# Kernel tuning notes

Hardware: AMD Instinct MI355X
Metric: run time of the kernel (lower is better)

## Reference

```python
import jax, jax.numpy as jnp
import numpy as np

HEAD_DIM = 64
NUM_Q_HEADS = 32
NUM_KV_HEADS = 8
ROPE_FREQ = 10000.0
EPS = 1e-6


def _rms_norm(x, gamma):
    # normalize over last dim (head_dim)
    var = jnp.mean(jnp.square(x), axis=-1, keepdims=True)
    return x * jax.lax.rsqrt(var + EPS) * gamma


def _rope_cos_sin(seq_len, dtype=jnp.float32):
    inv_freq = 1.0 / (ROPE_FREQ ** (jnp.arange(0, HEAD_DIM, 2, dtype=jnp.float32) / HEAD_DIM))
    pos = jnp.arange(seq_len, dtype=jnp.float32)
    freqs = pos[:, None] * inv_freq[None, :]          # [S, hd/2]
    emb = jnp.concatenate([freqs, freqs], axis=-1)    # [S, hd]
    return jnp.cos(emb).astype(dtype), jnp.sin(emb).astype(dtype)


def _rotate_half(x):
    x1, x2 = jnp.split(x, 2, axis=-1)
    return jnp.concatenate([-x2, x1], axis=-1)


def _apply_rope(x, cos, sin):
    # x: [B, H, S, hd]; cos/sin: [S, hd]
    return x * cos[None, None, :, :] + _rotate_half(x) * sin[None, None, :, :]


def setup_inputs() -> dict:
    key = jax.random.key(0)
    ks = jax.random.split(key, 5)
    B, S, D = 2, 2048, 2048
    qkv_out = (NUM_Q_HEADS + 2 * NUM_KV_HEADS) * HEAD_DIM  # 3072
    x = jax.random.normal(ks[0], (B, S, D), dtype=jnp.float32)
    w_qkv = jax.random.normal(ks[1], (qkv_out, D), dtype=jnp.float32) * (D ** -0.5)
    w_out = jax.random.normal(ks[2], (D, NUM_Q_HEADS * HEAD_DIM), dtype=jnp.float32) * ((NUM_Q_HEADS * HEAD_DIM) ** -0.5)
    q_gamma = jnp.ones((HEAD_DIM,), dtype=jnp.float32)
    k_gamma = jnp.ones((HEAD_DIM,), dtype=jnp.float32)
    return {"x": x, "w_qkv": w_qkv, "w_out": w_out, "q_gamma": q_gamma, "k_gamma": k_gamma}


def reference(x, w_qkv, w_out, q_gamma, k_gamma):
    B, S, D = x.shape
    groups = NUM_Q_HEADS // NUM_KV_HEADS
    # fused QKV projection (no bias)
    qkv = jnp.einsum("bsd,od->bso", x, w_qkv)
    qkv = qkv.reshape(B, S, NUM_Q_HEADS + 2 * NUM_KV_HEADS, HEAD_DIM)
    qkv = jnp.transpose(qkv, (0, 2, 1, 3))  # [B, heads, S, hd]
    q = qkv[:, :NUM_Q_HEADS]
    k = qkv[:, NUM_Q_HEADS:NUM_Q_HEADS + NUM_KV_HEADS]
    v = qkv[:, NUM_Q_HEADS + NUM_KV_HEADS:]
    # QK RMSNorm over head_dim
    q = _rms_norm(q, q_gamma)
    k = _rms_norm(k, k_gamma)
    # RoPE
    cos, sin = _rope_cos_sin(S, dtype=x.dtype)
    q = _apply_rope(q, cos, sin)
    k = _apply_rope(k, cos, sin)
    # GQA: repeat-interleave kv heads
    k = jnp.repeat(k, groups, axis=1)
    v = jnp.repeat(v, groups, axis=1)
    # causal SDPA
    scale = HEAD_DIM ** -0.5
    scores = jnp.einsum("bhqd,bhkd->bhqk", q, k) * scale
    causal = jnp.tril(jnp.ones((S, S), dtype=bool))
    scores = jnp.where(causal[None, None], scores, jnp.finfo(scores.dtype).min)
    attn = jax.nn.softmax(scores, axis=-1)
    ctx = jnp.einsum("bhqk,bhkd->bhqd", attn, v)
    ctx = jnp.transpose(ctx, (0, 2, 1, 3)).reshape(B, S, NUM_Q_HEADS * HEAD_DIM)
    out = jnp.einsum("bsf,df->bsd", ctx, w_out)
    return out
```

## Files before the change

kernel.cpp:

```cpp
#include <hip/hip_runtime.h>

typedef _Float16 f16;
typedef __fp16 fp16x2 __attribute__((ext_vector_type(2)));
typedef _Float16 f16x8 __attribute__((ext_vector_type(8)));
typedef float f32x4 __attribute__((ext_vector_type(4)));
typedef float f32x16 __attribute__((ext_vector_type(16)));

#define AS1 __attribute__((address_space(1)))
#define AS3 __attribute__((address_space(3)))

#define SCALE_L2E 0.18033688011112042f


__device__ __forceinline__ void gload16(const void* g, void* l) {
    __builtin_amdgcn_global_load_lds(
        (const AS1 unsigned*)(unsigned long long)g,
        (AS3 unsigned*)(unsigned)(unsigned long long)l,
        16, 0, 0);
}

__device__ __forceinline__ unsigned pk2(float a, float b) {
    union { fp16x2 v; unsigned u; } c;
    c.v = __builtin_amdgcn_cvt_pkrtz(a, b);
    return c.u;
}

#define BAR() do { asm volatile("" ::: "memory"); __builtin_amdgcn_s_barrier(); asm volatile("" ::: "memory"); } while (0)


__global__ __launch_bounds__(256) void k_cast_all(const float* __restrict__ x,
                                                  const float* __restrict__ wq,
                                                  const float* __restrict__ wo,
                                                  f16* __restrict__ Xh,
                                                  f16* __restrict__ Wqh,
                                                  f16* __restrict__ Woh) {
    int i = (blockIdx.x * 256 + threadIdx.x) * 4;
    const float* src; f16* dst;
    if (i < 8388608)        { src = x  + i;            dst = Xh  + i; }
    else if (i < 14680064)  { src = wq + (i - 8388608); dst = Wqh + (i - 8388608); }
    else                    { src = wo + (i - 14680064); dst = Woh + (i - 14680064); }
    float4 v = *(const float4*)src;
    union { f16 h[4]; ushort4 u; } c;
    c.h[0] = (f16)v.x; c.h[1] = (f16)v.y; c.h[2] = (f16)v.z; c.h[3] = (f16)v.w;
    *(ushort4*)dst = c.u;
}


__global__ __launch_bounds__(256) void k_tab(float* __restrict__ cosT,
                                             float* __restrict__ sinT) {
    int idx = blockIdx.x * 256 + threadIdx.x;
    int s = idx >> 5, i = idx & 31;
    float ang = (float)s * exp2f(-(float)i * 0.4152410118609190f);
    cosT[idx] = cosf(ang);
    sinT[idx] = sinf(ang);
}


template <typename OutT, int BH>
__global__ __launch_bounds__(512, 2) void k_gemm256(const f16* __restrict__ A,
                                                    const f16* __restrict__ Bt,
                                                    OutT* __restrict__ C,
                                                    int M, int N, int K) {
    constexpr int BUFSZ = 32768 + BH * 16384;
    constexpr int NN = 2 * BH;
    __shared__ __align__(16) char sm[2 * BUFSZ];
    const int tid = threadIdx.x;
    const int lane = tid & 63, wid = tid >> 6;
    const int wm = wid >> 2, wn = wid & 3;
    const int lr = lane & 15, g4 = lane >> 4;
    const int m0 = blockIdx.y * 256, n0 = blockIdx.x * (128 * BH);
    const int NT = K >> 6;

    const int srow = tid >> 3;
    const int scol = ((tid & 7) ^ (srow & 7)) * 8;
    const f16* gA = A  + (size_t)(m0 + srow) * K + scol;
    const f16* gB = Bt + (size_t)(n0 + srow) * K + scol;

    auto STGA = [&](int t, int h) {
        char* d = sm + (t & 1) * BUFSZ + h * 16384 + tid * 16;
        gload16(gA + (size_t)(h * 128) * K + t * 64,      d);
        gload16(gA + (size_t)(h * 128 + 64) * K + t * 64, d + 8192);
    };
    auto STGB = [&](int t, int h) {
        char* d = sm + (t & 1) * BUFSZ + 32768 + h * 16384 + tid * 16;
        gload16(gB + (size_t)(h * 128) * K + t * 64,      d);
        gload16(gB + (size_t)(h * 128 + 64) * K + t * 64, d + 8192);
    };

    f32x4 acc[8][NN] = {};
    f16x8 bfr[NN][2];

    STGA(0, 0); STGA(0, 1); STGB(0, 0); if (BH == 2) STGB(0, 1);
    STGA(1, 0); STGA(1, 1); STGB(1, 0); if (BH == 2) STGB(1, 1);
    if constexpr (BH == 2) asm volatile("s_waitcnt vmcnt(8)" ::: "memory");
    else                   asm volatile("s_waitcnt vmcnt(6)" ::: "memory");
    BAR();

    for (int t = 0; t < NT; ++t) {
        const int buf = t & 1;
        const char* bA = sm + buf * BUFSZ + wm * 16384;
        const char* bB = sm + buf * BUFSZ + 32768 + (BH == 2 ? (wn >> 1) * 16384 : 0);
        const bool sA = (t >= 1) && (t + 1 < NT);
        const bool sB = (t + 2 < NT);
#pragma unroll
        for (int p = 0; p < 4; ++p) {
            f16x8 afr[2][2];
            if (p == 0) {
#pragma unroll
                for (int n = 0; n < NN; n++) {
                    const int r = (BH == 2 ? (wn & 1) * 64 : wn * 32) + n * 16 + lr;
#pragma unroll
                    for (int kk = 0; kk < 2; kk++)
                        bfr[n][kk] = *(const f16x8*)(bB + ((r * 128 + kk * 64 + g4 * 16) ^ ((r & 7) << 4)));
                }
            }
#pragma unroll
            for (int mm = 0; mm < 2; mm++) {
                const int r = (2 * p + mm) * 16 + lr;
#pragma unroll
                for (int kk = 0; kk < 2; kk++)
                    afr[mm][kk] = *(const f16x8*)(bA + ((r * 128 + kk * 64 + g4 * 16) ^ ((r & 7) << 4)));
            }
            if (p == 0 && sA) STGA(t + 1, 0);
            if (p == 1 && sA) STGA(t + 1, 1);
            if (p == 2 && sB) STGB(t + 2, 0);
            if (p == 3 && sB && BH == 2) STGB(t + 2, 1);
            BAR();
            asm volatile("s_waitcnt lgkmcnt(0)" ::: "memory");
            __builtin_amdgcn_s_setprio(1);
#pragma unroll
            for (int mm = 0; mm < 2; mm++)
#pragma unroll
                for (int n = 0; n < NN; n++) {
                    acc[2 * p + mm][n] = __builtin_amdgcn_mfma_f32_16x16x32_f16(afr[mm][0], bfr[n][0], acc[2 * p + mm][n], 0, 0, 0);
                    acc[2 * p + mm][n] = __builtin_amdgcn_mfma_f32_16x16x32_f16(afr[mm][1], bfr[n][1], acc[2 * p + mm][n], 0, 0, 0);
                }
            __builtin_amdgcn_s_setprio(0);
            if (p == 3 && t + 1 < NT) {
                if (t + 2 < NT) {
                    if constexpr (BH == 2) asm volatile("s_waitcnt vmcnt(4)" ::: "memory");
                    else                   asm volatile("s_waitcnt vmcnt(2)" ::: "memory");
                } else {
                    asm volatile("s_waitcnt vmcnt(0)" ::: "memory");
                }
            }
            BAR();
        }
    }

#pragma unroll
    for (int m = 0; m < 8; m++)
#pragma unroll
        for (int n = 0; n < NN; n++) {
            size_t base = (size_t)(m0 + wm * 128 + m * 16 + g4 * 4) * N + (n0 + wn * (32 * BH) + n * 16 + lr);
#pragma unroll
            for (int j = 0; j < 4; j++)
                C[base + (size_t)j * N] = (OutT)acc[m][n][j];
        }
}


__global__ __launch_bounds__(256) void k_qkv_post(const f16* __restrict__ qkv,
                                                  const float* __restrict__ qg,
                                                  const float* __restrict__ kg,
                                                  const float* __restrict__ cosT,
                                                  const float* __restrict__ sinT,
                                                  f16* __restrict__ Qf,
                                                  f16* __restrict__ Kf,
                                                  f16* __restrict__ Vf) {
    __shared__ f16 tl[4][8][72];
    const int tid = threadIdx.x, lane = tid & 63, wv = tid >> 6;
    const int gw = blockIdx.x * 4 + wv;
    const int b = gw / 12288;
    const int r0 = gw - b * 12288;
    const int head = r0 >> 8;
    const int sblk = r0 & 255;
    const int s0 = sblk * 8;
    const int s_loc = lane >> 3, ch = lane & 7;
    const int s = s0 + s_loc;

    f16x8 v = *(const f16x8*)&qkv[((size_t)b * 2048 + s) * 3072 + head * 64 + ch * 8];

    if (head < 40) {
        float vf[8];
#pragma unroll
        for (int j = 0; j < 8; j++) vf[j] = (float)v[j];
        float ss = 0.f;
#pragma unroll
        for (int j = 0; j < 8; j++) ss += vf[j] * vf[j];
        ss += __shfl_xor(ss, 1); ss += __shfl_xor(ss, 2); ss += __shfl_xor(ss, 4);
        float rinv = rsqrtf(ss * (1.0f / 64.0f) + 1e-6f);
        const float* gam = (head < 32 ? qg : kg) + ch * 8;
        float4 g0 = *(const float4*)gam, g1 = *(const float4*)(gam + 4);
        float gv[8] = {g0.x, g0.y, g0.z, g0.w, g1.x, g1.y, g1.z, g1.w};
        float xn[8], ot[8];
#pragma unroll
        for (int j = 0; j < 8; j++) xn[j] = vf[j] * rinv * gv[j];
#pragma unroll
        for (int j = 0; j < 8; j++) ot[j] = __shfl_xor(xn[j], 4);
        const int i0 = (ch & 3) * 8;
        float4 c0  = *(const float4*)&cosT[(s << 5) + i0];
        float4 c1  = *(const float4*)&cosT[(s << 5) + i0 + 4];
        float4 sn0 = *(const float4*)&sinT[(s << 5) + i0];
        float4 sn1 = *(const float4*)&sinT[(s << 5) + i0 + 4];
        float cs[8] = {c0.x, c0.y, c0.z, c0.w, c1.x, c1.y, c1.z, c1.w};
        float sn[8] = {sn0.x, sn0.y, sn0.z, sn0.w, sn1.x, sn1.y, sn1.z, sn1.w};
        float sgn = (ch < 4) ? -1.0f : 1.0f;
        float ov[8];
#pragma unroll
        for (int j = 0; j < 8; j++) ov[j] = xn[j] * cs[j] + sgn * ot[j] * sn[j];
        if (head < 32) {
#pragma unroll
            for (int j = 0; j < 8; j++) ov[j] *= SCALE_L2E;
        }
        uint4 o;
        o.x = pk2(ov[0], ov[1]); o.y = pk2(ov[2], ov[3]);
        o.z = pk2(ov[4], ov[5]); o.w = pk2(ov[6], ov[7]);
        const int t = s >> 5;
        const int lane2 = (s & 31) + ((ch & 1) << 5);
        const int c = ch >> 1;
        f16* dst = (head < 32)
            ? Qf + (((size_t)(b * 32 + head) * 256 + t * 4 + c) * 512 + lane2 * 8)
            : Kf + (((size_t)(b * 8 + head - 32) * 256 + t * 4 + c) * 512 + lane2 * 8);
        *(uint4*)dst = o;
    } else {
        const int kh = head - 40;
        *(f16x8*)&tl[wv][s_loc][ch * 8] = v;
        asm volatile("s_waitcnt lgkmcnt(0)" ::: "memory");
        f16x8 cv;
#pragma unroll
        for (int rr = 0; rr < 8; rr++) cv[rr] = tl[wv][rr][lane];
        const int d = lane, dh = d >> 5;
        const int t = s0 >> 5, c = (s0 >> 4) & 1, hv = (s0 >> 3) & 1;
        const int g = dh * 2 + c;
        f16* dst = Vf + (((size_t)(b * 8 + kh) * 256 + t * 4 + g) * 512
                         + ((d & 31) + (hv << 5)) * 8);
        *(f16x8*)dst = cv;
    }
}


struct AttnPart { f32x16 o0, o1; float l; };

__device__ __forceinline__ AttnPart attn_part(int qb, int par, int lane, int lq, int hi,
        const f16* __restrict__ Qfp, const f16* __restrict__ Kfp,
        const f16* __restrict__ Vfp) {
    f16x8 qf[4];
#pragma unroll
    for (int c = 0; c < 4; c++)
        qf[c] = *(const f16x8*)&Qfp[((size_t)qb * 4 + c) * 512 + lane * 8];

    AttnPart P;
    P.o0 = (f32x16){}; P.o1 = (f32x16){};
    float lrun = 0.0f;

    f16x8 kf[4], va[2], vb[2];
    if (par <= qb) {
#pragma unroll
        for (int c = 0; c < 4; c++)
            kf[c] = *(const f16x8*)&Kfp[((size_t)par * 4 + c) * 512 + lane * 8];
#pragma unroll
        for (int c = 0; c < 2; c++) {
            va[c] = *(const f16x8*)&Vfp[((size_t)par * 4 + c)     * 512 + lane * 8];
            vb[c] = *(const f16x8*)&Vfp[((size_t)par * 4 + 2 + c) * 512 + lane * 8];
        }
    }

    for (int kt = par; kt <= qb; kt += 2) {
        f32x16 st = {};
#pragma unroll
        for (int c = 0; c < 4; c++)
            st = __builtin_amdgcn_mfma_f32_32x32x16_f16(kf[c], qf[c], st, 0, 0, 0);

        if (kt + 2 <= qb) {
#pragma unroll
            for (int c = 0; c < 4; c++)
                kf[c] = *(const f16x8*)&Kfp[((size_t)(kt + 2) * 4 + c) * 512 + lane * 8];
        }

        if (kt == qb) {
#pragma unroll
            for (int r = 0; r < 16; r++) {
                int kvl = (r & 3) + ((r >> 2) << 3) + (hi << 2);
                if (kvl > lq) st[r] = -1e30f;
            }
        }

        unsigned X[8];
        float ps0 = 0.0f, ps1 = 0.0f;
#pragma unroll
        for (int j = 0; j < 8; j++) {
            float p0 = __builtin_amdgcn_exp2f(st[2 * j]);
            float p1 = __builtin_amdgcn_exp2f(st[2 * j + 1]);
            ps0 += p0; ps1 += p1;
            X[j] = pk2(p0, p1);
        }
        lrun += ps0 + ps1;

#pragma unroll
        for (int c = 0; c < 2; c++) {
            unsigned a0 = X[4 * c], a1 = X[4 * c + 1], a2 = X[4 * c + 2], a3 = X[4 * c + 3];
            asm volatile("v_permlane32_swap_b32 %0, %1" : "+v"(a0), "+v"(a2));
            asm volatile("v_permlane32_swap_b32 %0, %1" : "+v"(a1), "+v"(a3));
            union { unsigned u[4]; f16x8 v; } pb;
            pb.u[0] = a0; pb.u[1] = a1; pb.u[2] = a2; pb.u[3] = a3;
            P.o0 = __builtin_amdgcn_mfma_f32_32x32x16_f16(va[c], pb.v, P.o0, 0, 0, 0);
            P.o1 = __builtin_amdgcn_mfma_f32_32x32x16_f16(vb[c], pb.v, P.o1, 0, 0, 0);
        }
        if (kt + 2 <= qb) {
#pragma unroll
            for (int c = 0; c < 2; c++) {
                va[c] = *(const f16x8*)&Vfp[((size_t)(kt + 2) * 4 + c)     * 512 + lane * 8];
                vb[c] = *(const f16x8*)&Vfp[((size_t)(kt + 2) * 4 + 2 + c) * 512 + lane * 8];
            }
        }
    }

    P.l = lrun + __shfl_xor(lrun, 32);
    return P;
}

__global__ __launch_bounds__(128) void k_attn(const f16* __restrict__ Qf,
                                              const f16* __restrict__ Kf,
                                              const f16* __restrict__ Vf,
                                              f16* __restrict__ ctx) {
    __shared__ float ldsO[32][65];
    __shared__ float ldsL[32];
    const int tid = threadIdx.x;
    const int par = tid >> 6, lane = tid & 63;
    const int lq = lane & 31, hi = lane >> 5;
    const int bh = blockIdx.y, b = bh >> 5, h = bh & 31, kh = h >> 2;
    const int pj = blockIdx.x;

    const f16* Qfp = Qf + (size_t)(b * 32 + h) * 131072;
    const f16* Kfp = Kf + (size_t)(b * 8 + kh) * 131072;
    const f16* Vfp = Vf + (size_t)(b * 8 + kh) * 131072;
    f16*       ctxbase = ctx + (size_t)b * 2048 * 2048 + h * 64;

    const int qbs[2] = {pj, 63 - pj};
#pragma unroll
    for (int s = 0; s < 2; s++) {
        const int qb = qbs[s];
        AttnPart P = attn_part(qb, par, lane, lq, hi, Qfp, Kfp, Vfp);

        if (par == 1) {
            if (hi == 0) ldsL[lq] = P.l;
#pragma unroll
            for (int r = 0; r < 16; r++) {
                int d = (r & 3) + ((r >> 2) << 3) + (hi << 2);
                ldsO[lq][d]      = P.o0[r];
                ldsO[lq][d + 32] = P.o1[r];
            }
        }
        __syncthreads();
        if (par == 0) {
            float inv = 1.0f / (P.l + ldsL[lq]);
            unsigned* row = (unsigned*)(ctxbase + (size_t)(qb * 32 + lq) * 2048);
#pragma unroll
            for (int g = 0; g < 4; g++) {
                int d = 8 * g + 4 * hi;
                float c0 = (P.o0[4 * g]     + ldsO[lq][d])     * inv;
                float c1 = (P.o0[4 * g + 1] + ldsO[lq][d + 1]) * inv;
                float c2 = (P.o0[4 * g + 2] + ldsO[lq][d + 2]) * inv;
                float c3 = (P.o0[4 * g + 3] + ldsO[lq][d + 3]) * inv;
                uint2 a; a.x = pk2(c0, c1); a.y = pk2(c2, c3);
                *(uint2*)(row + 2 * hi + 4 * g) = a;
                float e0 = (P.o1[4 * g]     + ldsO[lq][d + 32]) * inv;
                float e1 = (P.o1[4 * g + 1] + ldsO[lq][d + 33]) * inv;
                float e2 = (P.o1[4 * g + 2] + ldsO[lq][d + 34]) * inv;
                float e3 = (P.o1[4 * g + 3] + ldsO[lq][d + 35]) * inv;
                uint2 e; e.x = pk2(e0, e1); e.y = pk2(e2, e3);
                *(uint2*)(row + 16 + 2 * hi + 4 * g) = e;
            }
        }
        __syncthreads();
    }
}


extern "C" void kernel_launch(void* const* d_in, const int* in_sizes, int n_in,
                              void* d_out, int out_size, void* d_ws, size_t ws_size,
                              hipStream_t stream) {
    const float* x     = (const float*)d_in[0];
    const float* w_qkv = (const float*)d_in[1];
    const float* w_out = (const float*)d_in[2];
    const float* qg    = (const float*)d_in[3];
    const float* kg    = (const float*)d_in[4];
    float* out = (float*)d_out;
    char* ws = (char*)d_ws;

    float* cosT = (float*)(ws);
    float* sinT = (float*)(ws + 262144);
    f16* Xh     = (f16*)(ws + 524288);
    f16* Wqkvh  = (f16*)(ws + 17301504);
    f16* Wouth  = (f16*)(ws + 29884416);
    f16* QKVh   = (f16*)(ws + 38273024);
    f16* Qfb    = (f16*)(ws + 63438848);
    f16* Kfb    = (f16*)(ws + 80216064);
    f16* Vfb    = (f16*)(ws + 84410368);
    f16* Ctxh   = (f16*)(ws + 88604672);

    k_cast_all<<<18432, 256, 0, stream>>>(x, w_qkv, w_out, Xh, Wqkvh, Wouth);
    k_tab<<<256, 256, 0, stream>>>(cosT, sinT);

    k_gemm256<f16, 2><<<dim3(12, 16), 512, 0, stream>>>(Xh, Wqkvh, QKVh, 4096, 3072, 2048);

    k_qkv_post<<<6144, 256, 0, stream>>>(QKVh, qg, kg, cosT, sinT, Qfb, Kfb, Vfb);

    k_attn<<<dim3(32, 64), 128, 0, stream>>>(Qfb, Kfb, Vfb, Ctxh);

    k_gemm256<float, 1><<<dim3(16, 16), 512, 0, stream>>>(Ctxh, Wouth, out, 4096, 2048, 2048);
}
```

Baseline: 202.1 us.

## Fuse RoPE table into cast kernel, remap GEMM workgroups, reorder MFMA k-loop

Folds the cos/sin table computation into the cast kernel as extra blocks, removing one kernel launch. Remaps GEMM workgroup indices with an XCD-aware interleave (lin&7 stride) so that neighbouring tiles land on the same chiplet and share L2. Restructures the inner GEMM loop to iterate k-halves in the outer phase, loading half as many B fragments and four A fragments per phase, which lowers register pressure, and moves both B stage loads to the last phase. The remap assumes the total workgroup count divides by 8, which holds for both grids used.

```diff
diff --git a/kernel.cpp b/kernel.cpp
--- a/kernel.cpp
+++ b/kernel.cpp
@@ -33,7 +33,17 @@
                                                   const float* __restrict__ wo,
                                                   f16* __restrict__ Xh,
                                                   f16* __restrict__ Wqh,
-                                                  f16* __restrict__ Woh) {
+                                                  f16* __restrict__ Woh,
+                                                  float* __restrict__ cosT,
+                                                  float* __restrict__ sinT) {
+    if (blockIdx.x >= 18432) {
+        int idx = (blockIdx.x - 18432) * 256 + threadIdx.x;
+        int s = idx >> 5, i = idx & 31;
+        float ang = (float)s * exp2f(-(float)i * 0.4152410118609190f);
+        cosT[idx] = cosf(ang);
+        sinT[idx] = sinf(ang);
+        return;
+    }
     int i = (blockIdx.x * 256 + threadIdx.x) * 4;
     const float* src; f16* dst;
     if (i < 8388608)        { src = x  + i;            dst = Xh  + i; }
@@ -43,16 +53,6 @@
     union { f16 h[4]; ushort4 u; } c;
     c.h[0] = (f16)v.x; c.h[1] = (f16)v.y; c.h[2] = (f16)v.z; c.h[3] = (f16)v.w;
     *(ushort4*)dst = c.u;
-}
-
-
-__global__ __launch_bounds__(256) void k_tab(float* __restrict__ cosT,
-                                             float* __restrict__ sinT) {
-    int idx = blockIdx.x * 256 + threadIdx.x;
-    int s = idx >> 5, i = idx & 31;
-    float ang = (float)s * exp2f(-(float)i * 0.4152410118609190f);
-    cosT[idx] = cosf(ang);
-    sinT[idx] = sinf(ang);
 }
 
 
@@ -68,7 +68,13 @@
     const int lane = tid & 63, wid = tid >> 6;
     const int wm = wid >> 2, wn = wid & 3;
     const int lr = lane & 15, g4 = lane >> 4;
-    const int m0 = blockIdx.y * 256, n0 = blockIdx.x * (128 * BH);
+
+    const int gx = gridDim.x;
+    const int nwg = gx * gridDim.y;
+    int lin = blockIdx.y * gx + blockIdx.x;
+    lin = (lin & 7) * (nwg >> 3) + (lin >> 3);
+    const int bx = lin % gx, by = lin / gx;
+    const int m0 = by * 256, n0 = bx * (128 * BH);
     const int NT = K >> 6;
 
     const int srow = tid >> 3;
@@ -88,7 +94,7 @@
     };
 
     f32x4 acc[8][NN] = {};
-    f16x8 bfr[NN][2];
+    f16x8 bfr[NN];
 
     STGA(0, 0); STGA(0, 1); STGB(0, 0); if (BH == 2) STGB(0, 1);
     STGA(1, 0); STGA(1, 1); STGB(1, 0); if (BH == 2) STGB(1, 1);
@@ -104,37 +110,31 @@
         const bool sB = (t + 2 < NT);
 #pragma unroll
         for (int p = 0; p < 4; ++p) {
-            f16x8 afr[2][2];
-            if (p == 0) {
+            const int kk = p >> 1, mh = p & 1;
+            f16x8 afr[4];
+            if (mh == 0) {
 #pragma unroll
                 for (int n = 0; n < NN; n++) {
                     const int r = (BH == 2 ? (wn & 1) * 64 : wn * 32) + n * 16 + lr;
-#pragma unroll
-                    for (int kk = 0; kk < 2; kk++)
-                        bfr[n][kk] = *(const f16x8*)(bB + ((r * 128 + kk * 64 + g4 * 16) ^ ((r & 7) << 4)));
+                    bfr[n] = *(const f16x8*)(bB + ((r * 128 + kk * 64 + g4 * 16) ^ ((r & 7) << 4)));
                 }
             }
 #pragma unroll
-            for (int mm = 0; mm < 2; mm++) {
-                const int r = (2 * p + mm) * 16 + lr;
-#pragma unroll
-                for (int kk = 0; kk < 2; kk++)
-                    afr[mm][kk] = *(const f16x8*)(bA + ((r * 128 + kk * 64 + g4 * 16) ^ ((r & 7) << 4)));
+            for (int i = 0; i < 4; i++) {
+                const int r = (mh * 4 + i) * 16 + lr;
+                afr[i] = *(const f16x8*)(bA + ((r * 128 + kk * 64 + g4 * 16) ^ ((r & 7) << 4)));
             }
             if (p == 0 && sA) STGA(t + 1, 0);
             if (p == 1 && sA) STGA(t + 1, 1);
-            if (p == 2 && sB) STGB(t + 2, 0);
-            if (p == 3 && sB && BH == 2) STGB(t + 2, 1);
+            if (p == 3 && sB) { STGB(t + 2, 0); if (BH == 2) STGB(t + 2, 1); }
             BAR();
             asm volatile("s_waitcnt lgkmcnt(0)" ::: "memory");
             __builtin_amdgcn_s_setprio(1);
 #pragma unroll
-            for (int mm = 0; mm < 2; mm++)
-#pragma unroll
-                for (int n = 0; n < NN; n++) {
-                    acc[2 * p + mm][n] = __builtin_amdgcn_mfma_f32_16x16x32_f16(afr[mm][0], bfr[n][0], acc[2 * p + mm][n], 0, 0, 0);
-                    acc[2 * p + mm][n] = __builtin_amdgcn_mfma_f32_16x16x32_f16(afr[mm][1], bfr[n][1], acc[2 * p + mm][n], 0, 0, 0);
-                }
+            for (int i = 0; i < 4; i++)
+#pragma unroll
+                for (int n = 0; n < NN; n++)
+                    acc[mh * 4 + i][n] = __builtin_amdgcn_mfma_f32_16x16x32_f16(afr[i], bfr[n], acc[mh * 4 + i][n], 0, 0, 0);
             __builtin_amdgcn_s_setprio(0);
             if (p == 3 && t + 1 < NT) {
                 if (t + 2 < NT) {
@@ -400,8 +400,7 @@
     f16* Vfb    = (f16*)(ws + 84410368);
     f16* Ctxh   = (f16*)(ws + 88604672);
 
-    k_cast_all<<<18432, 256, 0, stream>>>(x, w_qkv, w_out, Xh, Wqkvh, Wouth);
-    k_tab<<<256, 256, 0, stream>>>(cosT, sinT);
+    k_cast_all<<<18688, 256, 0, stream>>>(x, w_qkv, w_out, Xh, Wqkvh, Wouth, cosT, sinT);
 
     k_gemm256<f16, 2><<<dim3(12, 16), 512, 0, stream>>>(Xh, Wqkvh, QKVh, 4096, 3072, 2048);
 
```

New measurement: 198.2 us. About the same (-1.9%).
